# Performance work log

Hardware: AMD Instinct MI355X
Metric: run time of the kernel (lower is better)

The kernel has to match this reference:

```python
import math
import jax, jax.numpy as jnp
import numpy as np

B, L, DIM, H = 2, 2048, 1024, 16
D = DIM // H  # head_dim = 64
EPS = 1e-6


def setup_inputs() -> dict:
    key = jax.random.key(0)
    ks = jax.random.split(key, 5)
    s = 0.02
    return {
        "x": jax.random.normal(ks[0], (B, L, DIM), jnp.float32),
        "pe": jax.random.normal(ks[1], (B, 1, L, D // 2, 2, 2), jnp.float32),
        "w_qkv": jax.random.normal(ks[2], (DIM, 3 * DIM), jnp.float32) * s,
        "q_scale": jnp.ones((D,), jnp.float32),
        "k_scale": jnp.ones((D,), jnp.float32),
        "w_proj": jax.random.normal(ks[3], (DIM, DIM), jnp.float32) * s,
        "b_proj": jnp.zeros((DIM,), jnp.float32),
    }


def _rmsnorm(t, scale):
    # flax nnx.RMSNorm: x * rsqrt(mean(x^2) + eps) * scale, over last dim
    var = jnp.mean(jnp.square(t), axis=-1, keepdims=True)
    return t * jax.lax.rsqrt(var + EPS) * scale


def _apply_rope(t, pe):
    # t: [B,H,L,D]; pe: [B,1,L,D/2,2,2]
    t2 = t.reshape(*t.shape[:-1], D // 2, 1, 2)
    out = pe[..., 0] * t2[..., 0] + pe[..., 1] * t2[..., 1]  # [B,H,L,D/2,2]
    return out.reshape(t.shape)


def reference(x, pe, w_qkv, q_scale, k_scale, w_proj, b_proj):
    # fused QKV projection
    qkv = jnp.einsum('bld,de->ble', x, w_qkv)  # [B,L,3*DIM]
    qkv = qkv.reshape(B, L, 3, H, D).transpose(2, 0, 3, 1, 4)  # [3,B,H,L,D]
    q, k, v = qkv[0], qkv[1], qkv[2]
    # QK RMSNorm
    q = _rmsnorm(q, q_scale)
    k = _rmsnorm(k, k_scale)
    # RoPE via pe
    q = _apply_rope(q, pe)
    k = _apply_rope(k, pe)
    # scaled dot product attention
    scores = jnp.einsum('bhqd,bhkd->bhqk', q, k) / math.sqrt(D)
    attn = jax.nn.softmax(scores, axis=-1)
    o = jnp.einsum('bhqk,bhkd->bhqd', attn, v)  # [B,H,L,D]
    o = o.transpose(0, 2, 1, 3).reshape(B, L, DIM)  # B H L D -> B L (H D)
    # output projection
    return jnp.einsum('bld,de->ble', o, w_proj) + b_proj
```

## Files before the change

kernel.cpp:

```cpp
#include <hip/hip_runtime.h>
#include <math.h>

#define BB 2
#define LL 2048
#define DIMM 1024
#define HH 16
#define DD 64
#define QKV_N 3072

typedef unsigned short u16;
typedef unsigned int u32;
typedef __attribute__((ext_vector_type(8))) short short8;
typedef __attribute__((ext_vector_type(4))) float f32x4;

__device__ __forceinline__ float bf2f(u16 h) {
    unsigned u = ((unsigned)h) << 16;
    return __uint_as_float(u);
}
__device__ __forceinline__ u16 f2bf(float f) {
    unsigned u = __float_as_uint(f);
    u += 0x7fffu + ((u >> 16) & 1u);
    return (u16)(u >> 16);
}
__device__ __forceinline__ u32 pack_bf2(float lo, float hi) {
    u32 a = __float_as_uint(hi) + 0x8000u;
    u32 b = __float_as_uint(lo) + 0x8000u;
    return __builtin_amdgcn_perm(a, b, 0x07060302u);
}
__device__ __forceinline__ u32 cvtpk_bf2(float lo, float hi) {
    u32 r;
    asm("v_cvt_pk_bf16_f32 %0, %1, %2" : "=v"(r) : "v"(lo), "v"(hi));
    return r;
}
__device__ __forceinline__ void gload16(const u16* g, u16* l) {
    __builtin_amdgcn_global_load_lds(
        (const __attribute__((address_space(1))) void*)g,
        (__attribute__((address_space(3))) void*)l, 16, 0, 0);
}

__global__ __launch_bounds__(256) void conv_all(
    const float* __restrict__ X, u16* __restrict__ Af,
    const float* __restrict__ Wqkv, u16* __restrict__ Wqkvt,
    const float* __restrict__ Wproj, u16* __restrict__ Wprojt)
{
    const int tid = threadIdx.x;
    if (blockIdx.x < 2048) {
        const int g = blockIdx.x * 256 + tid;
        const int lane = g & 63;
        const int frag = g >> 6;
        const int rt = frag >> 5;
        const int kts = (frag >> 1) & 15;
        const int ks2 = frag & 1;
        const int R = rt * 16 + (lane & 15);
        const int k = kts * 64 + ks2 * 32 + ((lane >> 4) & 3) * 8;
        float4 a = *(const float4*)&X[(size_t)R * DIMM + k];
        float4 b = *(const float4*)&X[(size_t)R * DIMM + k + 4];
        u16 t[8] = {f2bf(a.x), f2bf(a.y), f2bf(a.z), f2bf(a.w),
                    f2bf(b.x), f2bf(b.y), f2bf(b.z), f2bf(b.w)};
        *(uint4*)&Af[(size_t)frag * 512 + lane * 8] = *(uint4*)t;
        return;
    }

    __shared__ u16 s[64][72];
    const bool isfrag = (blockIdx.x < 2816);
    const int idx = isfrag ? (blockIdx.x - 2048) : (blockIdx.x - 2816);
    const int k0 = (idx & 15) * 64;
    const int n0 = (idx >> 4) * 64;
    const float* W = isfrag ? Wqkv : Wproj;
    u16* Wt = isfrag ? Wqkvt : Wprojt;
    const int K = 1024;
    const int N = isfrag ? QKV_N : DIMM;

#pragma unroll
    for (int t = 0; t < 16; ++t) {
        int flat = t * 256 + tid;
        int kk = flat >> 6, nn = flat & 63;
        s[nn][kk] = f2bf(W[(size_t)(k0 + kk) * N + n0 + nn]);
    }
    __syncthreads();
    if (isfrag) {
        const int kts = k0 >> 6;
        const int kdiv = K >> 6;
#pragma unroll
        for (int t2 = 0; t2 < 2; ++t2) {
            int i2 = t2 * 256 + tid;
            int fpart = i2 >> 6, lane_s = i2 & 63;
            int ct = (n0 >> 4) + (fpart >> 1);
            int ks2 = fpart & 1;
            int nn = (fpart >> 1) * 16 + (lane_s & 15);
            int kk = ks2 * 32 + ((lane_s >> 4) & 3) * 8;
            *(uint4*)&Wt[((size_t)(ct * kdiv + kts) * 2 + ks2) * 512 + lane_s * 8]
                = *(const uint4*)&s[nn][kk];
        }
    } else {
#pragma unroll
        for (int t2 = 0; t2 < 2; ++t2) {
            int chunk = t2 * 256 + tid;
            int nn = chunk >> 3, kc = chunk & 7;
            *(uint4*)&Wt[(size_t)(n0 + nn) * K + k0 + kc * 8] = *(uint4*)&s[nn][kc * 8];
        }
    }
}

__global__ __launch_bounds__(256) void gemm_qkv_all(
    const u16* __restrict__ Af, const u16* __restrict__ Bf,
    u16* __restrict__ C, u16* __restrict__ kp, u16* __restrict__ vp,
    const float* __restrict__ pe,
    const float* __restrict__ qs, const float* __restrict__ ks)
{
    __shared__ u16 smem[9216];

    const int region = blockIdx.x >> 9;
    const int bid = blockIdx.x & 511;

    const int tid = threadIdx.x;
    const int wave = tid >> 6, lane = tid & 63;
    const int mIdx = lane & 15, quad = lane >> 4;
    const int xcd = bid & 7, lid = bid >> 3;
    const int m0 = (xcd * 4 + (lid >> 4)) * 128;
    const int nblk = lid & 15;
    const int n0 = region * 1024 + nblk * 64;

    const u16* abase = Af + ((size_t)((m0 >> 4) + 2 * wave)) * 16384 + lane * 8;
    const u16* bbase = Bf + ((size_t)(n0 >> 4)) * 16384 + lane * 8;

    f32x4 acc[2][4];
#pragma unroll
    for (int a = 0; a < 2; ++a)
#pragma unroll
        for (int b = 0; b < 4; ++b) acc[a][b] = (f32x4){0.f, 0.f, 0.f, 0.f};

    short8 aA[2], bA[4], aB[2], bB[4];
#pragma unroll
    for (int i = 0; i < 2; ++i) aA[i] = *(const short8*)&abase[(size_t)i * 16384];
#pragma unroll
    for (int i = 0; i < 4; ++i) bA[i] = *(const short8*)&bbase[(size_t)i * 16384];

    for (int t = 0; t < 16; ++t) {
        const size_t o1 = (size_t)t * 1024 + 512;
#pragma unroll
        for (int i = 0; i < 2; ++i) aB[i] = *(const short8*)&abase[(size_t)i * 16384 + o1];
#pragma unroll
        for (int i = 0; i < 4; ++i) bB[i] = *(const short8*)&bbase[(size_t)i * 16384 + o1];
        __builtin_amdgcn_sched_barrier(0);
#pragma unroll
        for (int mt = 0; mt < 2; ++mt)
#pragma unroll
            for (int nt = 0; nt < 4; ++nt)
                acc[mt][nt] = __builtin_amdgcn_mfma_f32_16x16x32_bf16(
                    aA[mt], bA[nt], acc[mt][nt], 0, 0, 0);
        __builtin_amdgcn_sched_barrier(0);
        if (t + 1 < 16) {
            const size_t o0 = (size_t)(t + 1) * 1024;
#pragma unroll
            for (int i = 0; i < 2; ++i) aA[i] = *(const short8*)&abase[(size_t)i * 16384 + o0];
#pragma unroll
            for (int i = 0; i < 4; ++i) bA[i] = *(const short8*)&bbase[(size_t)i * 16384 + o0];
        }
        __builtin_amdgcn_sched_barrier(0);
#pragma unroll
        for (int mt = 0; mt < 2; ++mt)
#pragma unroll
            for (int nt = 0; nt < 4; ++nt)
                acc[mt][nt] = __builtin_amdgcn_mfma_f32_16x16x32_bf16(
                    aB[mt], bB[nt], acc[mt][nt], 0, 0, 0);
        __builtin_amdgcn_sched_barrier(0);
    }

    const int b = m0 >> 11;
    const int ktb = (m0 & 2047) >> 6;
    const int bh = b * 16 + nblk;

    if (region == 2) {
#pragma unroll
        for (int mt = 0; mt < 2; ++mt) {
            const int tl0 = 32 * wave + 16 * mt + 4 * quad;
#pragma unroll
            for (int nt = 0; nt < 4; ++nt) {
                const int d = 16 * nt + mIdx;
                const int lblk = ((tl0 >> 6) * 4 + (d >> 4)) * 2 + ((tl0 >> 5) & 1);
                const int ln = (d & 15) + 16 * ((tl0 >> 3) & 3);
                uint2 pr;
                pr.x = pack_bf2(acc[mt][nt][0], acc[mt][nt][1]);
                pr.y = pack_bf2(acc[mt][nt][2], acc[mt][nt][3]);
                *(uint2*)&smem[lblk * 512 + ln * 8 + (tl0 & 7)] = pr;
            }
        }
        __syncthreads();
#pragma unroll
        for (int ktl = 0; ktl < 2; ++ktl) {
            u16* dst = vp + ((size_t)(bh * 32 + ktb + ktl) * 8) * 512;
            const u16* src = &smem[ktl * 8 * 512];
#pragma unroll
            for (int ps = 0; ps < 2; ++ps) {
                const int off = (ps * 256 + tid) * 8;
                *(uint4*)&dst[off] = *(const uint4*)&src[off];
            }
        }
    } else {
        const float* scv = (region == 0) ? qs : ks;
        const float pre = (region == 0) ? 0.18033688011112042f : 1.0f;
        float scl[4];
#pragma unroll
        for (int nt = 0; nt < 4; ++nt) scl[nt] = scv[16 * nt + mIdx];

#pragma unroll
        for (int mt = 0; mt < 2; ++mt) {
#pragma unroll
            for (int r = 0; r < 4; ++r) {
                float s = 0.f;
#pragma unroll
                for (int nt = 0; nt < 4; ++nt) {
                    float a = acc[mt][nt][r];
                    s += a * a;
                }
                s += __shfl_xor(s, 1);
                s += __shfl_xor(s, 2);
                s += __shfl_xor(s, 4);
                s += __shfl_xor(s, 8);
                float rn = rsqrtf(s * (1.f / 64.f) + 1e-6f);
                const int tl = 32 * wave + 16 * mt + 4 * quad + r;
                const int R = m0 + tl;
                size_t peo = (size_t)R * 128;
#pragma unroll
                for (int nt = 0; nt < 4; ++nt) {
                    const int d = 16 * nt + mIdx;
                    float v = acc[mt][nt][r] * rn * scl[nt];
                    float pp = __shfl_xor(v, 1);
                    float2 pw = *(const float2*)&pe[peo + 2 * d];
                    float e  = (mIdx & 1) ? pp : v;
                    float od = (mIdx & 1) ? v : pp;
                    u16 val = f2bf((pw.x * e + pw.y * od) * pre);
                    if (region == 0) {
                        smem[tl * 72 + d] = val;
                    } else {
                        const int lblk = ((tl >> 6) * 4 + ((tl >> 4) & 3)) * 2 + (d >> 5);
                        smem[lblk * 512 + ((tl & 15) + 16 * ((d >> 3) & 3)) * 8 + (d & 7)] = val;
                    }
                }
            }
        }
        __syncthreads();
        if (region == 0) {
            const int row = tid >> 1, half = tid & 1;
            u16* dst = C + (size_t)(m0 + row) * QKV_N + n0 + half * 32;
            const u16* src = &smem[row * 72 + half * 32];
#pragma unroll
            for (int c = 0; c < 4; ++c)
                *(uint4*)&dst[c * 8] = *(const uint4*)&src[c * 8];
        } else {
#pragma unroll
            for (int ktl = 0; ktl < 2; ++ktl) {
                u16* dst = kp + ((size_t)(bh * 32 + ktb + ktl) * 8) * 512;
                const u16* src = &smem[ktl * 8 * 512];
#pragma unroll
                for (int ps = 0; ps < 2; ++ps) {
                    const int off = (ps * 256 + tid) * 8;
                    *(uint4*)&dst[off] = *(const uint4*)&src[off];
                }
            }
        }
    }
}

__global__ __launch_bounds__(256) void gemm_proj(
    const u16* __restrict__ A, const u16* __restrict__ Bt,
    const float* __restrict__ bias, float* __restrict__ C)
{
    __shared__ u16 smem[2 * 12288];

    const int tid = threadIdx.x;
    const int wave = tid >> 6, lane = tid & 63;
    const int mIdx = lane & 15, quad = lane >> 4;
    const int wr = wave >> 1, wc = wave & 1;
    const int xcd = blockIdx.x & 7, lid = blockIdx.x >> 3;
    const int m0 = (xcd * 8 + (lid >> 3)) * 64;
    const int n0 = (lid & 7) * 128;
    const int N = DIMM, K = DIMM;
    const int lr = lane >> 3, lc = lane & 7;

    f32x4 acc[2][4];
#pragma unroll
    for (int a = 0; a < 2; ++a)
#pragma unroll
        for (int b = 0; b < 4; ++b) acc[a][b] = (f32x4){0.f, 0.f, 0.f, 0.f};

    auto stage = [&](int buf, int k0) {
        u16* sA = smem + buf * 12288;
        u16* sB = sA + 4096;
#pragma unroll
        for (int j = 0; j < 2; ++j) {
            int r0 = 16 * wave + 8 * j + lr;
            gload16(&A[(size_t)(m0 + r0) * K + k0 + 8 * (lc ^ lr)],
                    &sA[(16 * wave + 8 * j) * 64]);
        }
#pragma unroll
        for (int j = 0; j < 4; ++j) {
            int r0 = 32 * wave + 8 * j + lr;
            gload16(&Bt[(size_t)(n0 + r0) * K + k0 + 8 * (lc ^ lr)],
                    &sB[(32 * wave + 8 * j) * 64]);
        }
    };

    stage(0, 0);
    __syncthreads();
    int cur = 0;
    for (int t = 0; t < 16; ++t) {
        if (t + 1 < 16) stage(cur ^ 1, (t + 1) * 64);
        const u16* sA = smem + cur * 12288;
        const u16* sB = sA + 4096;
#pragma unroll
        for (int ks2 = 0; ks2 < 2; ++ks2) {
            short8 af[2], bfr[4];
#pragma unroll
            for (int mt = 0; mt < 2; ++mt) {
                int Ra = 32 * wr + 16 * mt + mIdx;
                af[mt] = *(const short8*)&sA[Ra * 64 + 8 * ((ks2 * 4 + quad) ^ (Ra & 7))];
            }
#pragma unroll
            for (int nt = 0; nt < 4; ++nt) {
                int Rb = 64 * wc + 16 * nt + mIdx;
                bfr[nt] = *(const short8*)&sB[Rb * 64 + 8 * ((ks2 * 4 + quad) ^ (Rb & 7))];
            }
#pragma unroll
            for (int mt = 0; mt < 2; ++mt)
#pragma unroll
                for (int nt = 0; nt < 4; ++nt)
                    acc[mt][nt] = __builtin_amdgcn_mfma_f32_16x16x32_bf16(
                        af[mt], bfr[nt], acc[mt][nt], 0, 0, 0);
        }
        __syncthreads();
        cur ^= 1;
    }

#pragma unroll
    for (int mt = 0; mt < 2; ++mt)
#pragma unroll
        for (int r = 0; r < 4; ++r) {
            int row = m0 + 32 * wr + 16 * mt + quad * 4 + r;
#pragma unroll
            for (int nt = 0; nt < 4; ++nt) {
                int col = n0 + 64 * wc + 16 * nt + mIdx;
                C[(size_t)row * N + col] = acc[mt][nt][r] + bias[col];
            }
        }
}

__global__ __launch_bounds__(256, 2) void attn_mfma(
    const u16* __restrict__ qkv, const u16* __restrict__ kp,
    const u16* __restrict__ vp, u16* __restrict__ o)
{
    __shared__ u16 sP[128 * 64];

    const int tid = threadIdx.x;
    const int wave = tid >> 6;
    const int lane = tid & 63;
    const int mIdx = lane & 15;
    const int quad = lane >> 4;
    const int m7 = mIdx & 7;

    const int bid = ((blockIdx.x & 7) << 6) | (blockIdx.x >> 3);
    const int bh = bid >> 4;
    const int qt = bid & 15;
    const int b = bh >> 4, h = bh & 15;
    const int q0 = qt * 128;

    const u16* kbase = kp + (size_t)bh * 32 * 4096 + lane * 8;
    const u16* vbase = vp + (size_t)bh * 32 * 4096 + lane * 8;

    short8 aq[2][2];
#pragma unroll
    for (int g = 0; g < 2; ++g) {
        const u16* qrow = qkv + (size_t)b * LL * QKV_N + h * 64
                          + (size_t)(q0 + 32 * wave + 16 * g + mIdx) * QKV_N;
        aq[g][0] = *(const short8*)&qrow[quad * 8];
        aq[g][1] = *(const short8*)&qrow[32 + quad * 8];
    }

    const short8 bones = {(short)0x3F80, (short)0x3F80, (short)0x3F80, (short)0x3F80,
                          (short)0x3F80, (short)0x3F80, (short)0x3F80, (short)0x3F80};

    f32x4 Oacc[2][4];
    f32x4 lac[2];
#pragma unroll
    for (int g = 0; g < 2; ++g) {
        lac[g] = (f32x4){0.f, 0.f, 0.f, 0.f};
#pragma unroll
        for (int nb = 0; nb < 4; ++nb) Oacc[g][nb] = (f32x4){0.f, 0.f, 0.f, 0.f};
    }

    const int o0 = 8 * (quad ^ m7);
    const int o1 = 8 * ((quad + 4) ^ m7);
    u16* sPr0 = &sP[(32 * wave + mIdx) * 64];
    u16* sPr1 = &sP[(32 * wave + 16 + mIdx) * 64];

    short8 kfA[8], kfB[8], vf[8];

#pragma unroll
    for (int f = 0; f < 8; ++f) kfA[f] = *(const short8*)&kbase[f * 512];

    auto body = [&](short8* KC, short8* KN, int kt) {
        const size_t tb = (size_t)kt * 4096;
#pragma unroll
        for (int f = 0; f < 8; ++f) vf[f] = *(const short8*)&vbase[tb + f * 512];
        if (kt < 31) {
#pragma unroll
            for (int f = 0; f < 8; ++f) KN[f] = *(const short8*)&kbase[tb + 4096 + f * 512];
        }
        __builtin_amdgcn_sched_barrier(0);

#pragma unroll
        for (int nb = 0; nb < 4; ++nb) {
            const int pofs = (16 * nb + 4 * quad) ^ (8 * m7);
#pragma unroll
            for (int g = 0; g < 2; ++g) {
                f32x4 st = (f32x4){0.f, 0.f, 0.f, 0.f};
                st = __builtin_amdgcn_mfma_f32_16x16x32_bf16(KC[nb * 2 + 0], aq[g][0], st, 0, 0, 0);
                st = __builtin_amdgcn_mfma_f32_16x16x32_bf16(KC[nb * 2 + 1], aq[g][1], st, 0, 0, 0);
                float p0 = exp2f(st[0]), p1 = exp2f(st[1]);
                float p2 = exp2f(st[2]), p3 = exp2f(st[3]);
                uint2 wp;
                wp.x = cvtpk_bf2(p0, p1);
                wp.y = cvtpk_bf2(p2, p3);
                *(uint2*)&((g == 0 ? sPr0 : sPr1)[pofs]) = wp;
            }
        }
        short8 pa00 = *(const short8*)&sPr0[o0];
        short8 pa01 = *(const short8*)&sPr0[o1];
        short8 pa10 = *(const short8*)&sPr1[o0];
        short8 pa11 = *(const short8*)&sPr1[o1];

        lac[0] = __builtin_amdgcn_mfma_f32_16x16x32_bf16(pa00, bones, lac[0], 0, 0, 0);
        lac[0] = __builtin_amdgcn_mfma_f32_16x16x32_bf16(pa01, bones, lac[0], 0, 0, 0);
        lac[1] = __builtin_amdgcn_mfma_f32_16x16x32_bf16(pa10, bones, lac[1], 0, 0, 0);
        lac[1] = __builtin_amdgcn_mfma_f32_16x16x32_bf16(pa11, bones, lac[1], 0, 0, 0);

        __builtin_amdgcn_s_setprio(1);
#pragma unroll
        for (int nb = 0; nb < 4; ++nb) {
            Oacc[0][nb] = __builtin_amdgcn_mfma_f32_16x16x32_bf16(pa00, vf[nb * 2 + 0], Oacc[0][nb], 0, 0, 0);
            Oacc[0][nb] = __builtin_amdgcn_mfma_f32_16x16x32_bf16(pa01, vf[nb * 2 + 1], Oacc[0][nb], 0, 0, 0);
            Oacc[1][nb] = __builtin_amdgcn_mfma_f32_16x16x32_bf16(pa10, vf[nb * 2 + 0], Oacc[1][nb], 0, 0, 0);
            Oacc[1][nb] = __builtin_amdgcn_mfma_f32_16x16x32_bf16(pa11, vf[nb * 2 + 1], Oacc[1][nb], 0, 0, 0);
        }
        __builtin_amdgcn_s_setprio(0);
    };

    for (int kt2 = 0; kt2 < 16; ++kt2) {
        body(kfA, kfB, 2 * kt2);
        body(kfB, kfA, 2 * kt2 + 1);
    }

#pragma unroll
    for (int g = 0; g < 2; ++g)
#pragma unroll
        for (int r = 0; r < 4; ++r) {
            float linv = 1.f / lac[g][r];
            const int rowg = b * LL + q0 + 32 * wave + 16 * g + quad * 4 + r;
#pragma unroll
            for (int nb = 0; nb < 4; ++nb) {
                o[(size_t)rowg * DIMM + h * 64 + 16 * nb + mIdx] =
                    f2bf(Oacc[g][nb][r] * linv);
            }
        }
}

extern "C" void kernel_launch(void* const* d_in, const int* in_sizes, int n_in,
                              void* d_out, int out_size, void* d_ws, size_t ws_size,
                              hipStream_t stream) {
    const float* x       = (const float*)d_in[0];
    const float* pe      = (const float*)d_in[1];
    const float* w_qkv   = (const float*)d_in[2];
    const float* q_scale = (const float*)d_in[3];
    const float* k_scale = (const float*)d_in[4];
    const float* w_proj  = (const float*)d_in[5];
    const float* b_proj  = (const float*)d_in[6];
    float* out = (float*)d_out;

    char* ws = (char*)d_ws;
    u16* qkv    = (u16*)ws;  ws += (size_t)4096 * 3072 * 2;
    u16* o      = (u16*)ws;  ws += (size_t)4096 * 1024 * 2;
    u16* xb     = (u16*)ws;  ws += (size_t)4096 * 1024 * 2;
    u16* wqkvt  = (u16*)ws;  ws += (size_t)3072 * 1024 * 2;
    u16* wprojt = (u16*)ws;  ws += (size_t)1024 * 1024 * 2;
    u16* kpack  = (u16*)ws;  ws += (size_t)32 * 32 * 4096 * 2;
    u16* vpack  = (u16*)ws;  ws += (size_t)32 * 32 * 4096 * 2;

    conv_all<<<3072, 256, 0, stream>>>(x, xb, w_qkv, wqkvt, w_proj, wprojt);

    gemm_qkv_all<<<1536, 256, 0, stream>>>(
        xb, wqkvt, qkv, kpack, vpack, pe, q_scale, k_scale);

    attn_mfma<<<BB * HH * (LL / 128), 256, 0, stream>>>(qkv, kpack, vpack, o);

    gemm_proj<<<512, 256, 0, stream>>>(o, wprojt, b_proj, out);
}
```

Measured before the change: 197.1 us.

## Split attention over key halves and combine partial outputs in a separate kernel

Each attention block now processes only half of the key/value tiles, which doubles the grid to 1024 blocks. Each block writes unnormalized fp32 partial outputs and row sums to workspace. A new combine kernel adds the two halves, normalizes by the summed denominators and writes bf16. This is meant to expose more parallelism and balance work across CUs. In exchange it costs extra fp32 global traffic for the partials, plus one more kernel launch.

```diff
diff --git a/kernel.cpp b/kernel.cpp
--- a/kernel.cpp
+++ b/kernel.cpp
@@ -348,7 +348,7 @@
 
 __global__ __launch_bounds__(256, 2) void attn_mfma(
     const u16* __restrict__ qkv, const u16* __restrict__ kp,
-    const u16* __restrict__ vp, u16* __restrict__ o)
+    const u16* __restrict__ vp, float* __restrict__ Op, float* __restrict__ lp)
 {
     __shared__ u16 sP[128 * 64];
 
@@ -359,11 +359,14 @@
     const int quad = lane >> 4;
     const int m7 = mIdx & 7;
 
-    const int bid = ((blockIdx.x & 7) << 6) | (blockIdx.x >> 3);
-    const int bh = bid >> 4;
-    const int qt = bid & 15;
+    const int lbid = ((blockIdx.x & 7) << 7) | (blockIdx.x >> 3);
+    const int half = lbid & 1;
+    const int rest = lbid >> 1;
+    const int bh = rest >> 4;
+    const int qt = rest & 15;
     const int b = bh >> 4, h = bh & 15;
     const int q0 = qt * 128;
+    const int kt0 = half * 16;
 
     const u16* kbase = kp + (size_t)bh * 32 * 4096 + lane * 8;
     const u16* vbase = vp + (size_t)bh * 32 * 4096 + lane * 8;
@@ -397,13 +400,13 @@
     short8 kfA[8], kfB[8], vf[8];
 
 #pragma unroll
-    for (int f = 0; f < 8; ++f) kfA[f] = *(const short8*)&kbase[f * 512];
+    for (int f = 0; f < 8; ++f) kfA[f] = *(const short8*)&kbase[(size_t)kt0 * 4096 + f * 512];
 
     auto body = [&](short8* KC, short8* KN, int kt) {
         const size_t tb = (size_t)kt * 4096;
 #pragma unroll
         for (int f = 0; f < 8; ++f) vf[f] = *(const short8*)&vbase[tb + f * 512];
-        if (kt < 31) {
+        if (kt < kt0 + 15) {
 #pragma unroll
             for (int f = 0; f < 8; ++f) KN[f] = *(const short8*)&kbase[tb + 4096 + f * 512];
         }
@@ -446,23 +449,54 @@
         __builtin_amdgcn_s_setprio(0);
     };
 
-    for (int kt2 = 0; kt2 < 16; ++kt2) {
-        body(kfA, kfB, 2 * kt2);
-        body(kfB, kfA, 2 * kt2 + 1);
+    for (int kt2 = 0; kt2 < 8; ++kt2) {
+        body(kfA, kfB, kt0 + 2 * kt2);
+        body(kfB, kfA, kt0 + 2 * kt2 + 1);
     }
 
 #pragma unroll
     for (int g = 0; g < 2; ++g)
 #pragma unroll
         for (int r = 0; r < 4; ++r) {
-            float linv = 1.f / lac[g][r];
-            const int rowg = b * LL + q0 + 32 * wave + 16 * g + quad * 4 + r;
+            const int lrow = 32 * wave + 16 * g + quad * 4 + r;
+            const int rowg = b * LL + q0 + lrow;
 #pragma unroll
             for (int nb = 0; nb < 4; ++nb) {
-                o[(size_t)rowg * DIMM + h * 64 + 16 * nb + mIdx] =
-                    f2bf(Oacc[g][nb][r] * linv);
-            }
-        }
+                Op[((size_t)half * 4096 + rowg) * DIMM + h * 64 + 16 * nb + mIdx]
+                    = Oacc[g][nb][r];
+            }
+            if (mIdx == 0)
+                lp[((size_t)half * 512 + bh * 16 + qt) * 128 + lrow] = lac[g][r];
+        }
+}
+
+__global__ __launch_bounds__(256) void attn_combine(
+    const float* __restrict__ Op, const float* __restrict__ lp,
+    u16* __restrict__ o)
+{
+    const int rowg = blockIdx.x;
+    const int bb = rowg >> 11;
+    const int qt = (rowg >> 7) & 15;
+    const int lr = rowg & 127;
+
+    __shared__ float linv[16];
+    if (threadIdx.x < 16) {
+        const int h = threadIdx.x;
+        const size_t base = ((size_t)((bb * 16 + h) * 16 + qt)) * 128 + lr;
+        float l0 = lp[base];
+        float l1 = lp[base + 65536];
+        linv[h] = 1.f / (l0 + l1);
+    }
+    __syncthreads();
+
+    const int c = threadIdx.x * 4;
+    float4 a0 = *(const float4*)&Op[(size_t)rowg * DIMM + c];
+    float4 a1 = *(const float4*)&Op[(size_t)(4096 + rowg) * DIMM + c];
+    const float li = linv[c >> 6];
+    uint2 wp;
+    wp.x = cvtpk_bf2((a0.x + a1.x) * li, (a0.y + a1.y) * li);
+    wp.y = cvtpk_bf2((a0.z + a1.z) * li, (a0.w + a1.w) * li);
+    *(uint2*)&o[(size_t)rowg * DIMM + c] = wp;
 }
 
 extern "C" void kernel_launch(void* const* d_in, const int* in_sizes, int n_in,
@@ -485,13 +519,17 @@
     u16* wprojt = (u16*)ws;  ws += (size_t)1024 * 1024 * 2;
     u16* kpack  = (u16*)ws;  ws += (size_t)32 * 32 * 4096 * 2;
     u16* vpack  = (u16*)ws;  ws += (size_t)32 * 32 * 4096 * 2;
+    float* Opart = (float*)ws;  ws += (size_t)2 * 4096 * 1024 * 4;
+    float* lpart = (float*)ws;  ws += (size_t)2 * 512 * 128 * 4;
 
     conv_all<<<3072, 256, 0, stream>>>(x, xb, w_qkv, wqkvt, w_proj, wprojt);
 
     gemm_qkv_all<<<1536, 256, 0, stream>>>(
         xb, wqkvt, qkv, kpack, vpack, pe, q_scale, k_scale);
 
-    attn_mfma<<<BB * HH * (LL / 128), 256, 0, stream>>>(qkv, kpack, vpack, o);
+    attn_mfma<<<2 * BB * HH * (LL / 128), 256, 0, stream>>>(
+        qkv, kpack, vpack, Opart, lpart);
+    attn_combine<<<4096, 256, 0, stream>>>(Opart, lpart, o);
 
     gemm_proj<<<512, 256, 0, stream>>>(o, wprojt, b_proj, out);
 }
```

Result: slower. 212.2 us (+7.6%).

## Pack attention output and proj weights into MFMA fragment layout, drop LDS in proj GEMM

Applied to the files above, without the earlier changes.

The attention kernel now stages its normalized output through shared memory and writes it in an MFMA-fragment-packed layout. The proj weight conversion uses the same fragment packing as the QKV weights. gemm_proj then loads A and B fragments directly from global memory into registers with a two-stage register double buffer, removing LDS staging and block barriers. The risk is less data reuse across waves, since each wave loads its own fragments, and an extra LDS pass plus barrier at the end of the attention kernel.

```diff
diff --git a/kernel.cpp b/kernel.cpp
--- a/kernel.cpp
+++ b/kernel.cpp
@@ -31,11 +31,6 @@
     u32 r;
     asm("v_cvt_pk_bf16_f32 %0, %1, %2" : "=v"(r) : "v"(lo), "v"(hi));
     return r;
-}
-__device__ __forceinline__ void gload16(const u16* g, u16* l) {
-    __builtin_amdgcn_global_load_lds(
-        (const __attribute__((address_space(1))) void*)g,
-        (__attribute__((address_space(3))) void*)l, 16, 0, 0);
 }
 
 __global__ __launch_bounds__(256) void conv_all(
@@ -62,14 +57,13 @@
     }
 
     __shared__ u16 s[64][72];
-    const bool isfrag = (blockIdx.x < 2816);
-    const int idx = isfrag ? (blockIdx.x - 2048) : (blockIdx.x - 2816);
+    const bool isqkv = (blockIdx.x < 2816);
+    const int idx = isqkv ? (blockIdx.x - 2048) : (blockIdx.x - 2816);
     const int k0 = (idx & 15) * 64;
     const int n0 = (idx >> 4) * 64;
-    const float* W = isfrag ? Wqkv : Wproj;
-    u16* Wt = isfrag ? Wqkvt : Wprojt;
-    const int K = 1024;
-    const int N = isfrag ? QKV_N : DIMM;
+    const float* W = isqkv ? Wqkv : Wproj;
+    u16* Wt = isqkv ? Wqkvt : Wprojt;
+    const int N = isqkv ? QKV_N : DIMM;
 
 #pragma unroll
     for (int t = 0; t < 16; ++t) {
@@ -78,9 +72,8 @@
         s[nn][kk] = f2bf(W[(size_t)(k0 + kk) * N + n0 + nn]);
     }
     __syncthreads();
-    if (isfrag) {
+    {
         const int kts = k0 >> 6;
-        const int kdiv = K >> 6;
 #pragma unroll
         for (int t2 = 0; t2 < 2; ++t2) {
             int i2 = t2 * 256 + tid;
@@ -89,15 +82,8 @@
             int ks2 = fpart & 1;
             int nn = (fpart >> 1) * 16 + (lane_s & 15);
             int kk = ks2 * 32 + ((lane_s >> 4) & 3) * 8;
-            *(uint4*)&Wt[((size_t)(ct * kdiv + kts) * 2 + ks2) * 512 + lane_s * 8]
+            *(uint4*)&Wt[((size_t)(ct * 16 + kts) * 2 + ks2) * 512 + lane_s * 8]
                 = *(const uint4*)&s[nn][kk];
-        }
-    } else {
-#pragma unroll
-        for (int t2 = 0; t2 < 2; ++t2) {
-            int chunk = t2 * 256 + tid;
-            int nn = chunk >> 3, kc = chunk & 7;
-            *(uint4*)&Wt[(size_t)(n0 + nn) * K + k0 + kc * 8] = *(uint4*)&s[nn][kc * 8];
         }
     }
 }
@@ -264,20 +250,18 @@
 }
 
 __global__ __launch_bounds__(256) void gemm_proj(
-    const u16* __restrict__ A, const u16* __restrict__ Bt,
+    const u16* __restrict__ Of, const u16* __restrict__ Bf,
     const float* __restrict__ bias, float* __restrict__ C)
 {
-    __shared__ u16 smem[2 * 12288];
-
     const int tid = threadIdx.x;
     const int wave = tid >> 6, lane = tid & 63;
     const int mIdx = lane & 15, quad = lane >> 4;
-    const int wr = wave >> 1, wc = wave & 1;
     const int xcd = blockIdx.x & 7, lid = blockIdx.x >> 3;
-    const int m0 = (xcd * 8 + (lid >> 3)) * 64;
-    const int n0 = (lid & 7) * 128;
-    const int N = DIMM, K = DIMM;
-    const int lr = lane >> 3, lc = lane & 7;
+    const int m0 = (xcd * 4 + (lid >> 4)) * 128;
+    const int n0 = (lid & 15) * 64;
+
+    const u16* abase = Of + ((size_t)((m0 >> 4) + 2 * wave)) * 16384 + lane * 8;
+    const u16* bbase = Bf + ((size_t)(n0 >> 4)) * 16384 + lane * 8;
 
     f32x4 acc[2][4];
 #pragma unroll
@@ -285,70 +269,60 @@
 #pragma unroll
         for (int b = 0; b < 4; ++b) acc[a][b] = (f32x4){0.f, 0.f, 0.f, 0.f};
 
-    auto stage = [&](int buf, int k0) {
-        u16* sA = smem + buf * 12288;
-        u16* sB = sA + 4096;
-#pragma unroll
-        for (int j = 0; j < 2; ++j) {
-            int r0 = 16 * wave + 8 * j + lr;
-            gload16(&A[(size_t)(m0 + r0) * K + k0 + 8 * (lc ^ lr)],
-                    &sA[(16 * wave + 8 * j) * 64]);
-        }
-#pragma unroll
-        for (int j = 0; j < 4; ++j) {
-            int r0 = 32 * wave + 8 * j + lr;
-            gload16(&Bt[(size_t)(n0 + r0) * K + k0 + 8 * (lc ^ lr)],
-                    &sB[(32 * wave + 8 * j) * 64]);
-        }
-    };
-
-    stage(0, 0);
-    __syncthreads();
-    int cur = 0;
+    short8 aA[2], bA[4], aB[2], bB[4];
+#pragma unroll
+    for (int i = 0; i < 2; ++i) aA[i] = *(const short8*)&abase[(size_t)i * 16384];
+#pragma unroll
+    for (int i = 0; i < 4; ++i) bA[i] = *(const short8*)&bbase[(size_t)i * 16384];
+
     for (int t = 0; t < 16; ++t) {
-        if (t + 1 < 16) stage(cur ^ 1, (t + 1) * 64);
-        const u16* sA = smem + cur * 12288;
-        const u16* sB = sA + 4096;
-#pragma unroll
-        for (int ks2 = 0; ks2 < 2; ++ks2) {
-            short8 af[2], bfr[4];
-#pragma unroll
-            for (int mt = 0; mt < 2; ++mt) {
-                int Ra = 32 * wr + 16 * mt + mIdx;
-                af[mt] = *(const short8*)&sA[Ra * 64 + 8 * ((ks2 * 4 + quad) ^ (Ra & 7))];
-            }
-#pragma unroll
-            for (int nt = 0; nt < 4; ++nt) {
-                int Rb = 64 * wc + 16 * nt + mIdx;
-                bfr[nt] = *(const short8*)&sB[Rb * 64 + 8 * ((ks2 * 4 + quad) ^ (Rb & 7))];
-            }
-#pragma unroll
-            for (int mt = 0; mt < 2; ++mt)
-#pragma unroll
-                for (int nt = 0; nt < 4; ++nt)
-                    acc[mt][nt] = __builtin_amdgcn_mfma_f32_16x16x32_bf16(
-                        af[mt], bfr[nt], acc[mt][nt], 0, 0, 0);
-        }
-        __syncthreads();
-        cur ^= 1;
-    }
-
+        const size_t o1 = (size_t)t * 1024 + 512;
+#pragma unroll
+        for (int i = 0; i < 2; ++i) aB[i] = *(const short8*)&abase[(size_t)i * 16384 + o1];
+#pragma unroll
+        for (int i = 0; i < 4; ++i) bB[i] = *(const short8*)&bbase[(size_t)i * 16384 + o1];
+        __builtin_amdgcn_sched_barrier(0);
+#pragma unroll
+        for (int mt = 0; mt < 2; ++mt)
+#pragma unroll
+            for (int nt = 0; nt < 4; ++nt)
+                acc[mt][nt] = __builtin_amdgcn_mfma_f32_16x16x32_bf16(
+                    aA[mt], bA[nt], acc[mt][nt], 0, 0, 0);
+        __builtin_amdgcn_sched_barrier(0);
+        if (t + 1 < 16) {
+            const size_t o0 = (size_t)(t + 1) * 1024;
+#pragma unroll
+            for (int i = 0; i < 2; ++i) aA[i] = *(const short8*)&abase[(size_t)i * 16384 + o0];
+#pragma unroll
+            for (int i = 0; i < 4; ++i) bA[i] = *(const short8*)&bbase[(size_t)i * 16384 + o0];
+        }
+        __builtin_amdgcn_sched_barrier(0);
+#pragma unroll
+        for (int mt = 0; mt < 2; ++mt)
+#pragma unroll
+            for (int nt = 0; nt < 4; ++nt)
+                acc[mt][nt] = __builtin_amdgcn_mfma_f32_16x16x32_bf16(
+                    aB[mt], bB[nt], acc[mt][nt], 0, 0, 0);
+        __builtin_amdgcn_sched_barrier(0);
+    }
+
+    float bv[4];
+#pragma unroll
+    for (int nt = 0; nt < 4; ++nt) bv[nt] = bias[n0 + 16 * nt + mIdx];
 #pragma unroll
     for (int mt = 0; mt < 2; ++mt)
 #pragma unroll
         for (int r = 0; r < 4; ++r) {
-            int row = m0 + 32 * wr + 16 * mt + quad * 4 + r;
-#pragma unroll
-            for (int nt = 0; nt < 4; ++nt) {
-                int col = n0 + 64 * wc + 16 * nt + mIdx;
-                C[(size_t)row * N + col] = acc[mt][nt][r] + bias[col];
-            }
+            const int row = m0 + 32 * wave + 16 * mt + 4 * quad + r;
+#pragma unroll
+            for (int nt = 0; nt < 4; ++nt)
+                C[(size_t)row * DIMM + n0 + 16 * nt + mIdx] = acc[mt][nt][r] + bv[nt];
         }
 }
 
 __global__ __launch_bounds__(256, 2) void attn_mfma(
     const u16* __restrict__ qkv, const u16* __restrict__ kp,
-    const u16* __restrict__ vp, u16* __restrict__ o)
+    const u16* __restrict__ vp, u16* __restrict__ Of)
 {
     __shared__ u16 sP[128 * 64];
 
@@ -455,14 +429,27 @@
     for (int g = 0; g < 2; ++g)
 #pragma unroll
         for (int r = 0; r < 4; ++r) {
-            float linv = 1.f / lac[g][r];
-            const int rowg = b * LL + q0 + 32 * wave + 16 * g + quad * 4 + r;
+            const float linv = 1.f / lac[g][r];
+            const int lane2 = 4 * quad + r;
 #pragma unroll
             for (int nb = 0; nb < 4; ++nb) {
-                o[(size_t)rowg * DIMM + h * 64 + 16 * nb + mIdx] =
-                    f2bf(Oacc[g][nb][r] * linv);
-            }
-        }
+                const int d = 16 * nb + mIdx;
+                const int lanep = lane2 + 16 * ((2 * nb + (mIdx >> 3)) & 3);
+                sP[((2 * wave + g) * 2 + (nb >> 1)) * 512 + lanep * 8 + (mIdx & 7)]
+                    = f2bf(Oacc[g][nb][r] * linv);
+            }
+        }
+    __syncthreads();
+    {
+        const int rt0 = (b * LL + q0) >> 4;
+#pragma unroll
+        for (int ps = 0; ps < 4; ++ps) {
+            const int idx = ps * 256 + tid;
+            const int lfrag = idx >> 6, within = idx & 63;
+            const size_t gfrag = (size_t)(rt0 + (lfrag >> 1)) * 32 + h * 2 + (lfrag & 1);
+            *(uint4*)&Of[gfrag * 512 + within * 8] = *(const uint4*)&sP[lfrag * 512 + within * 8];
+        }
+    }
 }
 
 extern "C" void kernel_launch(void* const* d_in, const int* in_sizes, int n_in,
@@ -479,7 +466,7 @@
 
     char* ws = (char*)d_ws;
     u16* qkv    = (u16*)ws;  ws += (size_t)4096 * 3072 * 2;
-    u16* o      = (u16*)ws;  ws += (size_t)4096 * 1024 * 2;
+    u16* of     = (u16*)ws;  ws += (size_t)4096 * 1024 * 2;
     u16* xb     = (u16*)ws;  ws += (size_t)4096 * 1024 * 2;
     u16* wqkvt  = (u16*)ws;  ws += (size_t)3072 * 1024 * 2;
     u16* wprojt = (u16*)ws;  ws += (size_t)1024 * 1024 * 2;
@@ -491,7 +478,7 @@
     gemm_qkv_all<<<1536, 256, 0, stream>>>(
         xb, wqkvt, qkv, kpack, vpack, pe, q_scale, k_scale);
 
-    attn_mfma<<<BB * HH * (LL / 128), 256, 0, stream>>>(qkv, kpack, vpack, o);
-
-    gemm_proj<<<512, 256, 0, stream>>>(o, wprojt, b_proj, out);
-}
+    attn_mfma<<<BB * HH * (LL / 128), 256, 0, stream>>>(qkv, kpack, vpack, of);
+
+    gemm_proj<<<512, 256, 0, stream>>>(of, wprojt, b_proj, out);
+}
```

New measurement: 199.3 us. No clear change (+1.1%).
